# Optimization experiments

Measured on AMD Instinct MI355X. Metric: run time of the kernel, lower is better.

Reference implementation:

```python
import jax, jax.numpy as jnp
import numpy as np

FP8_MAX = 448.0
FP8_HI_PREC_MAX = 224.0
UNC_THRESH = 0.1
EPS = 1e-08


def setup_inputs() -> dict:
    key = jax.random.key(0)
    k1, k2, k3 = jax.random.split(key, 3)
    B, S, H, D, M = 1, 4096, 32, 128, 4096
    return {
        "k": jax.random.normal(k1, (B, S, H, D), dtype=jnp.float32),
        "v": jax.random.normal(k2, (B, S, H, D), dtype=jnp.float32),
        "uncertainty": jax.random.uniform(k3, (B, S), dtype=jnp.float32),
        "k_cache": jnp.zeros((H, M, D), dtype=jnp.float32),
        "v_cache": jnp.zeros((H, M, D), dtype=jnp.float32),
        "k_scales": jnp.ones((H, M), dtype=jnp.float32),
        "v_scales": jnp.ones((H, M), dtype=jnp.float32),
        "current_pos": 0,
    }


def reference(k, v, uncertainty, k_cache, v_cache, k_scales, v_scales, current_pos):
    # k, v: [1, S, H, D]; caches: [H, M, D]; scales: [H, M]
    H, M, D = k_cache.shape
    S = k.shape[1]
    pos = (current_pos + jnp.arange(S)) % M  # circular-buffer write positions

    kt = k[0]  # [S, H, D]
    vt = v[0]

    # per-token fp8 divisor: high-precision range when uncertain
    div = jnp.where(uncertainty[0] > UNC_THRESH, FP8_HI_PREC_MAX, FP8_MAX)  # [S]

    # per-token amax over all heads and dims -> scalar scale per token
    k_s = jnp.maximum(jnp.max(jnp.abs(kt), axis=(1, 2)) / div, EPS)  # [S]
    v_s = jnp.maximum(jnp.max(jnp.abs(vt), axis=(1, 2)) / div, EPS)

    kq = jnp.clip(kt / k_s[:, None, None], -FP8_MAX, FP8_MAX)  # [S, H, D]
    vq = jnp.clip(vt / v_s[:, None, None], -FP8_MAX, FP8_MAX)

    # scatter-append into circular buffer ([H, S, D] layout for cache writes)
    new_k_cache = k_cache.at[:, pos].set(jnp.swapaxes(kq, 0, 1))
    new_v_cache = v_cache.at[:, pos].set(jnp.swapaxes(vq, 0, 1))
    new_k_scales = k_scales.at[:, pos].set(jnp.broadcast_to(k_s, (H, S)))
    new_v_scales = v_scales.at[:, pos].set(jnp.broadcast_to(v_s, (H, S)))
    return (new_k_cache, new_v_cache, new_k_scales, new_v_scales)
```

## Files before the change

kernel.cpp:

```cpp
#include <hip/hip_runtime.h>

#define HH 32
#define DD 128
#define MM 4096
#define ROW_F4 1024
#define D_F4   32

typedef float v4f __attribute__((ext_vector_type(4)));

__global__ __launch_bounds__(64)
void teleport_quant_kernel(const float* __restrict__ kin,
                           const float* __restrict__ vin,
                           const float* __restrict__ unc,
                           const float* __restrict__ kc_in,
                           const float* __restrict__ vc_in,
                           const float* __restrict__ ksc_in,
                           const float* __restrict__ vsc_in,
                           const int*   __restrict__ cur_pos,
                           float* __restrict__ kc_out,
                           float* __restrict__ vc_out,
                           float* __restrict__ ksc_out,
                           float* __restrict__ vsc_out,
                           int S)
{
    const int lane = threadIdx.x;
    const int w    = blockIdx.x;
    const int m    = w >> 1;
    const int isV  = w & 1;

    int cp  = *cur_pos;
    int cpm = cp % MM; if (cpm < 0) cpm += MM;
    int s0  = m - cpm; if (s0 < 0) s0 += MM;
    const int s = (s0 < S) ? (s0 + MM * ((S - 1 - s0) / MM)) : -1;

    const v4f* cin  = reinterpret_cast<const v4f*>(isV ? vc_in : kc_in);
    v4f*       cout = reinterpret_cast<v4f*>(isV ? vc_out : kc_out);
    const float* sin_ = isV ? vsc_in  : ksc_in;
    float*       sout = isV ? vsc_out : ksc_out;

    if (s < 0) {
        #pragma unroll
        for (int c = 0; c < 16; ++c) {
            int f4 = c * 64 + lane;
            int o  = (f4 >> 5) * (MM * D_F4) + m * D_F4 + (f4 & 31);
            cout[o] = cin[o];
        }
        if (lane < HH) sout[lane * MM + m] = sin_[lane * MM + m];
        return;
    }

    const v4f* src = reinterpret_cast<const v4f*>(isV ? vin : kin)
                     + (size_t)s * ROW_F4;

    v4f a[16];
    float am = 0.0f;
    #pragma unroll
    for (int c = 0; c < 16; ++c) {
        a[c] = src[c * 64 + lane];
        am = fmaxf(am, fmaxf(fmaxf(fabsf(a[c].x), fabsf(a[c].y)),
                             fmaxf(fabsf(a[c].z), fabsf(a[c].w))));
    }

    #pragma unroll
    for (int off = 32; off > 0; off >>= 1)
        am = fmaxf(am, __shfl_xor(am, off, 64));

    const float u   = unc[s];
    const float div = (u > 0.1f) ? 224.0f : 448.0f;
    const float sc  = fmaxf(am / div, 1e-8f);
    const float r   = 1.0f / sc;

    #pragma unroll
    for (int c = 0; c < 16; ++c) {
        int f4 = c * 64 + lane;
        int o  = (f4 >> 5) * (MM * D_F4) + m * D_F4 + (f4 & 31);
        v4f q;
        q.x = fminf(fmaxf(a[c].x * r, -448.0f), 448.0f);
        q.y = fminf(fmaxf(a[c].y * r, -448.0f), 448.0f);
        q.z = fminf(fmaxf(a[c].z * r, -448.0f), 448.0f);
        q.w = fminf(fmaxf(a[c].w * r, -448.0f), 448.0f);
        cout[o] = q;
    }

    if (lane < HH) sout[lane * MM + m] = sc;
}

extern "C" void kernel_launch(void* const* d_in, const int* in_sizes, int n_in,
                              void* d_out, int out_size, void* d_ws, size_t ws_size,
                              hipStream_t stream) {
    const float* kin = (const float*)d_in[0];
    const float* vin = (const float*)d_in[1];
    const float* unc = (const float*)d_in[2];
    const float* kc  = (const float*)d_in[3];
    const float* vc  = (const float*)d_in[4];
    const float* ksc = (const float*)d_in[5];
    const float* vsc = (const float*)d_in[6];
    const int*   cp  = (const int*)d_in[7];
    const int S = in_sizes[2];

    float* out  = (float*)d_out;
    float* kco  = out;
    float* vco  = kco + (size_t)HH * MM * DD;
    float* ksco = vco + (size_t)HH * MM * DD;
    float* vsco = ksco + (size_t)HH * MM;

    teleport_quant_kernel<<<2 * MM, 64, 0, stream>>>(
        kin, vin, unc, kc, vc, ksc, vsc, cp, kco, vco, ksco, vsco, S);
}
```

Before: 48.19 us.

## Process four rows per block with double-buffered register loads

Each 64-thread block now handles four cache rows instead of one. It uses two register buffers so the next row's load is issued before the current row is quantized and stored. The aim is more memory-level parallelism per wave and less per-block launch overhead. In exchange the grid is four times smaller, register pressure roughly doubles, and occupancy drops.

```diff
diff --git a/kernel.cpp b/kernel.cpp
--- a/kernel.cpp
+++ b/kernel.cpp
@@ -8,7 +8,90 @@
 
 typedef float v4f __attribute__((ext_vector_type(4)));
 
-__global__ __launch_bounds__(64)
+struct RowCtx {
+    int m, s;
+    const v4f*  src;
+    const v4f*  cin;
+    v4f*        cout;
+    const float* sin_;
+    float*       sout;
+};
+
+__device__ __forceinline__ RowCtx make_row(int r, int cpm, int S,
+    const float* kin, const float* vin,
+    const float* kc_in, const float* vc_in,
+    const float* ksc_in, const float* vsc_in,
+    float* kc_out, float* vc_out, float* ksc_out, float* vsc_out)
+{
+    RowCtx R;
+    R.m = r >> 1;
+    const int isV = r & 1;
+    int s0 = R.m - cpm; if (s0 < 0) s0 += MM;
+    R.s = (s0 < S) ? (s0 + MM * ((S - 1 - s0) / MM)) : -1;
+    R.src  = (R.s >= 0)
+           ? reinterpret_cast<const v4f*>(isV ? vin : kin) + (size_t)R.s * ROW_F4
+           : nullptr;
+    R.cin  = reinterpret_cast<const v4f*>(isV ? vc_in : kc_in);
+    R.cout = reinterpret_cast<v4f*>(isV ? vc_out : kc_out);
+    R.sin_ = isV ? vsc_in  : ksc_in;
+    R.sout = isV ? vsc_out : ksc_out;
+    return R;
+}
+
+__device__ __forceinline__ void row_load(v4f (&a)[16], const RowCtx& R, int lane)
+{
+    if (R.s >= 0) {
+        #pragma unroll
+        for (int c = 0; c < 16; ++c) a[c] = R.src[c * 64 + lane];
+    } else {
+        #pragma unroll
+        for (int c = 0; c < 16; ++c) {
+            int f4 = c * 64 + lane;
+            a[c] = R.cin[(f4 >> 5) * (MM * D_F4) + R.m * D_F4 + (f4 & 31)];
+        }
+    }
+}
+
+__device__ __forceinline__ void row_proc(v4f (&a)[16], const RowCtx& R, int lane,
+                                         const float* __restrict__ unc)
+{
+    if (R.s >= 0) {
+        float am = 0.0f;
+        #pragma unroll
+        for (int c = 0; c < 16; ++c)
+            am = fmaxf(am, fmaxf(fmaxf(fabsf(a[c].x), fabsf(a[c].y)),
+                                 fmaxf(fabsf(a[c].z), fabsf(a[c].w))));
+        #pragma unroll
+        for (int off = 32; off > 0; off >>= 1)
+            am = fmaxf(am, __shfl_xor(am, off, 64));
+        const float u   = unc[R.s];
+        const float div = (u > 0.1f) ? 224.0f : 448.0f;
+        const float sc  = fmaxf(am / div, 1e-8f);
+        const float rr  = 1.0f / sc;
+        #pragma unroll
+        for (int c = 0; c < 16; ++c) {
+            int f4 = c * 64 + lane;
+            int o  = (f4 >> 5) * (MM * D_F4) + R.m * D_F4 + (f4 & 31);
+            v4f q;
+            q.x = fminf(fmaxf(a[c].x * rr, -448.0f), 448.0f);
+            q.y = fminf(fmaxf(a[c].y * rr, -448.0f), 448.0f);
+            q.z = fminf(fmaxf(a[c].z * rr, -448.0f), 448.0f);
+            q.w = fminf(fmaxf(a[c].w * rr, -448.0f), 448.0f);
+            R.cout[o] = q;
+        }
+        if (lane < HH) R.sout[lane * MM + R.m] = sc;
+    } else {
+        #pragma unroll
+        for (int c = 0; c < 16; ++c) {
+            int f4 = c * 64 + lane;
+            int o  = (f4 >> 5) * (MM * D_F4) + R.m * D_F4 + (f4 & 31);
+            R.cout[o] = a[c];
+        }
+        if (lane < HH) R.sout[lane * MM + R.m] = R.sin_[lane * MM + R.m];
+    }
+}
+
+__global__ __launch_bounds__(64, 2)
 void teleport_quant_kernel(const float* __restrict__ kin,
                            const float* __restrict__ vin,
                            const float* __restrict__ unc,
@@ -25,64 +108,28 @@
 {
     const int lane = threadIdx.x;
     const int w    = blockIdx.x;
-    const int m    = w >> 1;
-    const int isV  = w & 1;
 
     int cp  = *cur_pos;
     int cpm = cp % MM; if (cpm < 0) cpm += MM;
-    int s0  = m - cpm; if (s0 < 0) s0 += MM;
-    const int s = (s0 < S) ? (s0 + MM * ((S - 1 - s0) / MM)) : -1;
 
-    const v4f* cin  = reinterpret_cast<const v4f*>(isV ? vc_in : kc_in);
-    v4f*       cout = reinterpret_cast<v4f*>(isV ? vc_out : kc_out);
-    const float* sin_ = isV ? vsc_in  : ksc_in;
-    float*       sout = isV ? vsc_out : ksc_out;
+    const RowCtx R0 = make_row(4 * w + 0, cpm, S, kin, vin, kc_in, vc_in,
+                               ksc_in, vsc_in, kc_out, vc_out, ksc_out, vsc_out);
+    const RowCtx R1 = make_row(4 * w + 1, cpm, S, kin, vin, kc_in, vc_in,
+                               ksc_in, vsc_in, kc_out, vc_out, ksc_out, vsc_out);
+    const RowCtx R2 = make_row(4 * w + 2, cpm, S, kin, vin, kc_in, vc_in,
+                               ksc_in, vsc_in, kc_out, vc_out, ksc_out, vsc_out);
+    const RowCtx R3 = make_row(4 * w + 3, cpm, S, kin, vin, kc_in, vc_in,
+                               ksc_in, vsc_in, kc_out, vc_out, ksc_out, vsc_out);
 
-    if (s < 0) {
-        #pragma unroll
-        for (int c = 0; c < 16; ++c) {
-            int f4 = c * 64 + lane;
-            int o  = (f4 >> 5) * (MM * D_F4) + m * D_F4 + (f4 & 31);
-            cout[o] = cin[o];
-        }
-        if (lane < HH) sout[lane * MM + m] = sin_[lane * MM + m];
-        return;
-    }
-
-    const v4f* src = reinterpret_cast<const v4f*>(isV ? vin : kin)
-                     + (size_t)s * ROW_F4;
-
-    v4f a[16];
-    float am = 0.0f;
-    #pragma unroll
-    for (int c = 0; c < 16; ++c) {
-        a[c] = src[c * 64 + lane];
-        am = fmaxf(am, fmaxf(fmaxf(fabsf(a[c].x), fabsf(a[c].y)),
-                             fmaxf(fabsf(a[c].z), fabsf(a[c].w))));
-    }
-
-    #pragma unroll
-    for (int off = 32; off > 0; off >>= 1)
-        am = fmaxf(am, __shfl_xor(am, off, 64));
-
-    const float u   = unc[s];
-    const float div = (u > 0.1f) ? 224.0f : 448.0f;
-    const float sc  = fmaxf(am / div, 1e-8f);
-    const float r   = 1.0f / sc;
-
-    #pragma unroll
-    for (int c = 0; c < 16; ++c) {
-        int f4 = c * 64 + lane;
-        int o  = (f4 >> 5) * (MM * D_F4) + m * D_F4 + (f4 & 31);
-        v4f q;
-        q.x = fminf(fmaxf(a[c].x * r, -448.0f), 448.0f);
-        q.y = fminf(fmaxf(a[c].y * r, -448.0f), 448.0f);
-        q.z = fminf(fmaxf(a[c].z * r, -448.0f), 448.0f);
-        q.w = fminf(fmaxf(a[c].w * r, -448.0f), 448.0f);
-        cout[o] = q;
-    }
-
-    if (lane < HH) sout[lane * MM + m] = sc;
+    v4f A[16], B[16];
+    row_load(A, R0, lane);
+    row_load(B, R1, lane);
+    row_proc(A, R0, lane, unc);
+    row_load(A, R2, lane);
+    row_proc(B, R1, lane, unc);
+    row_load(B, R3, lane);
+    row_proc(A, R2, lane, unc);
+    row_proc(B, R3, lane, unc);
 }
 
 extern "C" void kernel_launch(void* const* d_in, const int* in_sizes, int n_in,
@@ -104,6 +151,6 @@
     float* ksco = vco + (size_t)HH * MM * DD;
     float* vsco = ksco + (size_t)HH * MM;
 
-    teleport_quant_kernel<<<2 * MM, 64, 0, stream>>>(
+    teleport_quant_kernel<<<(2 * MM) / 4, 64, 0, stream>>>(
         kin, vin, unc, kc, vc, ksc, vsc, cp, kco, vco, ksco, vsco, S);
 }
```

Result: slower. 50.82 us (+5.5%).
